# Kernel tuning notes

Hardware: AMD Instinct MI355X
Metric: run time of the kernel (lower is better)

## Reference

```python
import jax, jax.numpy as jnp
import numpy as np
import math

N_HEAD = 16


def _alibi_slopes(n_head):
    def get_slopes(n):
        start = 2.0 ** (-2.0 ** (-(math.log2(n) - 3)))
        return [start * start ** i for i in range(n)]
    if math.log2(n_head).is_integer():
        slopes = get_slopes(n_head)
    else:
        c = 2 ** math.floor(math.log2(n_head))
        slopes = get_slopes(c)
        extra = get_slopes(2 * c)[0::2]
        slopes = slopes + extra[: n_head - c]
    return np.asarray(slopes, dtype=np.float32)


def setup_inputs() -> dict:
    key = jax.random.key(0)
    ks = jax.random.split(key, 9)
    B, S, E = 2, 2048, 1024
    sd = 1.0 / math.sqrt(E)
    inp = {
        "x": jax.random.normal(ks[0], (B, S, E), jnp.float32),
        "Wq": jax.random.uniform(ks[1], (E, E), jnp.float32, -sd, sd),
        "bq": jnp.zeros((E,), jnp.float32),
        "Wk": jax.random.uniform(ks[2], (E, E), jnp.float32, -sd, sd),
        "bk": jnp.zeros((E,), jnp.float32),
        "Wv": jax.random.uniform(ks[3], (E, E), jnp.float32, -sd, sd),
        "bv": jnp.zeros((E,), jnp.float32),
        "Wo": jax.random.uniform(ks[4], (E, E), jnp.float32, -sd, sd),
        "bo": jnp.zeros((E,), jnp.float32),
        "alibi_slopes": jnp.asarray(_alibi_slopes(N_HEAD)),
    }
    return inp


def reference(x, Wq, bq, Wk, bk, Wv, bv, Wo, bo, alibi_slopes):
    B, S, E = x.shape
    H = N_HEAD
    hd = E // H
    scale = hd ** -0.5
    # Linear layers (torch Linear: y = x @ W.T + b)
    Q = (x @ Wq.T + bq).reshape(B, H, S, hd)  # faithful: view, NOT transpose
    K = (x @ Wk.T + bk).reshape(B, H, S, hd)
    V = (x @ Wv.T + bv).reshape(B, H, S, hd)
    scores = jnp.einsum("bhqd,bhkd->bhqk", Q, K) * scale
    pos = jnp.arange(S)
    rel = jnp.abs(pos[None, :] - pos[:, None]).astype(scores.dtype)  # [S,S]
    bias = alibi_slopes[None, :, None, None] * rel[None, None]  # [1,H,S,S]
    scores = scores - bias
    probs = jax.nn.softmax(scores, axis=-1)
    # faithful quirk: keep only head index 1's probs, broadcast to all heads
    probs1 = probs[:, 1:2, :, :]  # [B,1,S,S]
    attn_out = jnp.matmul(probs1, V)  # broadcast -> [B,H,S,hd]
    attn_out = attn_out.reshape(B, S, E)
    out = attn_out @ Wo.T + bo
    return (out, probs1)
```

## Files before the change

### kernel.cpp

```cpp
#include <hip/hip_runtime.h>

typedef __bf16 bf16;
typedef __bf16 bf16_4 __attribute__((ext_vector_type(4)));
typedef __bf16 bf16_8 __attribute__((ext_vector_type(8)));
typedef float f32_4 __attribute__((ext_vector_type(4)));

#define GLDS16(g, l) \
  __builtin_amdgcn_global_load_lds((const __attribute__((address_space(1))) unsigned int*)(g), \
                                   (__attribute__((address_space(3))) unsigned int*)(l), 16, 0, 0)

__global__ __launch_bounds__(256) void convert_all(
    const float* __restrict__ x, const float* __restrict__ wq, const float* __restrict__ wk,
    const float* __restrict__ wv, const float* __restrict__ wo,
    bf16* __restrict__ xb, bf16* __restrict__ wqb, bf16* __restrict__ wkb,
    bf16* __restrict__ wvb, bf16* __restrict__ wob)
{
    for (int i = blockIdx.x * 256 + threadIdx.x; i < 2097152; i += 2048 * 256) {
        const float* s; bf16* d; int off;
        if (i < 1048576) { s = x; d = xb; off = i; }
        else {
            int j = i - 1048576;
            int sel = j >> 18;
            off = j & 262143;
            s = (sel == 0) ? wq : (sel == 1) ? wk : (sel == 2) ? wv : wo;
            d = (sel == 0) ? wqb : (sel == 1) ? wkb : (sel == 2) ? wvb : wob;
        }
        float4 v = reinterpret_cast<const float4*>(s)[off];
        bf16_4 o; o.x = (bf16)v.x; o.y = (bf16)v.y; o.z = (bf16)v.z; o.w = (bf16)v.w;
        reinterpret_cast<bf16_4*>(d)[off] = o;
    }
}

template<int BM, int KU, int NW>
__device__ __forceinline__ void gemm_core(
    const bf16* __restrict__ Ab, int lda,
    const bf16* __restrict__ Wb, int ldw,
    int K, int m0, int n0, int tid,
    bf16* As, bf16* Bs,
    f32_4 (&acc)[(BM == 128) ? 4 : 2][(BM == 128) ? 4 : 2])
{
    constexpr int MI = (BM == 128) ? 4 : 2;
    constexpr int NJ = (BM == 128) ? 4 : 2;
    constexpr int ITA = (BM * 8) / (NW * 64);
    constexpr int ITB = 1024 / (NW * 64);
    const int lane = tid & 63;
    const int wave = tid >> 6;
    const int l15  = lane & 15;
    const int quad = lane >> 4;
    const int WM = (BM == 128) ? (wave >> 1) * 64 : (wave >> 2) * 32;
    const int WN = (BM == 128) ? (wave & 1) * 64 : (wave & 3) * 32;

#pragma unroll
    for (int i = 0; i < MI; i++)
#pragma unroll
        for (int j = 0; j < NJ; j++) acc[i][j] = (f32_4)(0.0f);

    for (int k0 = 0; k0 < K; k0 += 64 * KU) {
#pragma unroll
        for (int ku = 0; ku < KU; ++ku) {
            bf16* Asu = As + ku * BM * 64;
            bf16* Bsu = Bs + ku * 128 * 64;
            int kk = k0 + ku * 64;
#pragma unroll
            for (int it = 0; it < ITA; ++it) {
                int p = wave * (BM * 8 / NW) + it * 64 + lane;
                int r = p >> 3;
                int q = (p & 7) ^ (r & 7);
                GLDS16(Ab + (long long)(m0 + r) * lda + kk + q * 8, Asu + p * 8);
            }
#pragma unroll
            for (int it = 0; it < ITB; ++it) {
                int p = wave * (1024 / NW) + it * 64 + lane;
                int r = p >> 3;
                int q = (p & 7) ^ (r & 7);
                GLDS16(Wb + (long long)(n0 + r) * ldw + kk + q * 8, Bsu + p * 8);
            }
        }
        __syncthreads();

#pragma unroll
        for (int ku = 0; ku < KU; ++ku) {
            bf16* Asu = As + ku * BM * 64;
            bf16* Bsu = Bs + ku * 128 * 64;
#pragma unroll
            for (int kh = 0; kh < 2; ++kh) {
                bf16_8 af[MI], bfr[NJ];
#pragma unroll
                for (int t = 0; t < MI; ++t) {
                    int r = WM + t * 16 + l15;
                    int q = (kh * 4 + quad) ^ (r & 7);
                    af[t] = *reinterpret_cast<const bf16_8*>(&Asu[r * 64 + q * 8]);
                }
#pragma unroll
                for (int j = 0; j < NJ; ++j) {
                    int r = WN + j * 16 + l15;
                    int q = (kh * 4 + quad) ^ (r & 7);
                    bfr[j] = *reinterpret_cast<const bf16_8*>(&Bsu[r * 64 + q * 8]);
                }
#pragma unroll
                for (int i = 0; i < MI; ++i)
#pragma unroll
                    for (int j = 0; j < NJ; ++j)
                        acc[i][j] = __builtin_amdgcn_mfma_f32_16x16x32_bf16(af[i], bfr[j], acc[i][j], 0, 0, 0);
            }
        }
        __syncthreads();
    }
}

__global__ __launch_bounds__(512) void proj_merged(
    const bf16* __restrict__ x_bf,
    const bf16* __restrict__ wv_bf, const float* __restrict__ bv, bf16* __restrict__ v_bf,
    const bf16* __restrict__ wq_bf, const float* __restrict__ bq, bf16* __restrict__ qh1,
    const bf16* __restrict__ wk_bf, const float* __restrict__ bk, bf16* __restrict__ kh1)
{
    __shared__ alignas(16) bf16 As[64 * 64 * 2];
    __shared__ alignas(16) bf16 Bs[128 * 64 * 2];
    const int tid = threadIdx.x;
    const int lane = tid & 63, wave = tid >> 6, l15 = lane & 15, quad = lane >> 4;
    const int n0 = blockIdx.x * 128;

    int m0;
    const bf16* Ab; const bf16* Wb; const float* bvec; bf16* op;
    long long obase;
    int y = blockIdx.y;
    if (y < 64) { m0 = y * 64; Ab = x_bf; Wb = wv_bf; bvec = bv; op = v_bf; obase = 0; }
    else {
        int sub = y - 64;
        int batch = (sub >> 1) & 1;
        int sel = sub >> 2;
        m0 = (sub & 1) * 64;
        Ab = x_bf + (long long)batch * 2097152LL + 131072LL;
        Wb = sel ? wk_bf : wq_bf;
        bvec = sel ? bk : bq;
        op = sel ? kh1 : qh1;
        obase = (long long)batch * 131072LL;
    }

    f32_4 acc[2][2];
    gemm_core<64, 2, 8>(Ab, 1024, Wb, 1024, 1024, m0, n0, tid, As, Bs, acc);

    const int WM = (wave >> 2) * 32;
    const int WN = (wave & 3) * 32;
#pragma unroll
    for (int i = 0; i < 2; i++)
#pragma unroll
        for (int j = 0; j < 2; j++)
#pragma unroll
            for (int rg = 0; rg < 4; rg++) {
                int m = m0 + WM + i * 16 + quad * 4 + rg;
                int n = n0 + WN + j * 16 + l15;
                op[obase + (long long)m * 1024 + n] = (bf16)(acc[i][j][rg] + bvec[n]);
            }
}

__global__ __launch_bounds__(256) void scores_tr(
    const bf16* __restrict__ qh1, const bf16* __restrict__ kh1,
    const float* __restrict__ slopes,
    bf16* __restrict__ pb, float* __restrict__ spart,
    const unsigned short* __restrict__ v_bf, unsigned short* __restrict__ vt)
{
    __shared__ alignas(16) char smem[32768];
    bf16* As = (bf16*)smem;
    bf16* Bs = (bf16*)(smem + 16384);
    const int tid = threadIdx.x;
    const int lane = tid & 63, wave = tid >> 6, l15 = lane & 15, quad = lane >> 4;
    const int n0 = blockIdx.x * 128;
    const int m0 = blockIdx.y * 128;
    const int z  = blockIdx.z;

    f32_4 acc[4][4];
    gemm_core<128, 1, 4>(qh1 + (long long)z * 131072LL, 64,
                         kh1 + (long long)z * 131072LL, 64, 64, m0, n0, tid, As, Bs, acc);

    const int WM = (wave >> 1) * 64;
    const int WN = (wave & 1) * 64;
    const float slope = slopes[1];
    long long obase = (long long)z * 4194304LL;
#pragma unroll
    for (int i = 0; i < 4; i++) {
#pragma unroll
        for (int rg = 0; rg < 4; rg++) {
            int m = m0 + WM + i * 16 + quad * 4 + rg;
            float rowpart = 0.0f;
#pragma unroll
            for (int j = 0; j < 4; j++) {
                int n = n0 + WN + j * 16 + l15;
                float v = acc[i][j][rg] * 0.125f - slope * fabsf((float)(m - n));
                float e = __expf(v);
                rowpart += e;
                pb[obase + (long long)m * 2048 + n] = (bf16)e;
            }
            rowpart += __shfl_xor(rowpart, 1, 64);
            rowpart += __shfl_xor(rowpart, 2, 64);
            rowpart += __shfl_xor(rowpart, 4, 64);
            rowpart += __shfl_xor(rowpart, 8, 64);
            if (l15 == 0)
                spart[((long long)z * 2048 + m) * 32 + (n0 >> 6) + (WN >> 6)] = rowpart;
        }
    }

    unsigned short* tile = (unsigned short*)smem;
    int flat = z * 256 + blockIdx.y * 16 + blockIdx.x;
#pragma unroll
    for (int uu = 0; uu < 2; ++uu) {
        int u = flat * 2 + uu;
        int k0 = (u & 31) * 64, h = (u >> 5) & 15, b = u >> 9;
        const unsigned short* src = v_bf + (long long)b * 2097152LL + (long long)h * 131072LL;
#pragma unroll
        for (int p = 0; p < 8; p++) {
            int idx = tid + p * 256;
            int k = idx >> 5, dc = idx & 31;
            ushort2 w = *reinterpret_cast<const ushort2*>(&src[(long long)(k0 + k) * 64 + dc * 2]);
            tile[(dc * 2) * 66 + k]     = w.x;
            tile[(dc * 2 + 1) * 66 + k] = w.y;
        }
        __syncthreads();
        unsigned short* dst = vt + (long long)b * 2097152LL + (long long)h * 64 * 2048LL + k0;
#pragma unroll
        for (int p = 0; p < 8; p++) {
            int idx = tid + p * 256;
            int d = idx >> 5, kc = idx & 31;
            ushort2 w;
            w.x = tile[d * 66 + kc * 2];
            w.y = tile[d * 66 + kc * 2 + 1];
            *reinterpret_cast<ushort2*>(&dst[(long long)d * 2048 + kc * 2]) = w;
        }
        __syncthreads();
    }
}

__global__ __launch_bounds__(512) void pv_fused(
    const bf16* __restrict__ pb, const bf16* __restrict__ vt,
    const float* __restrict__ spart,
    bf16* __restrict__ attn, float* __restrict__ probs_f)
{
    __shared__ alignas(16) bf16 As[64 * 64 * 2];
    __shared__ alignas(16) bf16 Bs[128 * 64 * 2];
    __shared__ float rs[64];
    const int tid = threadIdx.x;
    const int lane = tid & 63, wave = tid >> 6, l15 = lane & 15, quad = lane >> 4;
    const int nx = blockIdx.x;
    const int n0 = nx * 128;
    const int m0 = blockIdx.y * 64;
    const int z  = blockIdx.z;

    {
        int r = tid >> 3, part = tid & 7;
        const float* sp = spart + ((long long)z * 2048 + m0 + r) * 32 + part * 4;
        float4 a = *reinterpret_cast<const float4*>(sp);
        float v = a.x + a.y + a.z + a.w;
        v += __shfl_xor(v, 1, 64);
        v += __shfl_xor(v, 2, 64);
        v += __shfl_xor(v, 4, 64);
        if (part == 0) rs[r] = 1.0f / v;
    }
    __syncthreads();

    const bf16* Ab = pb + (long long)z * 4194304LL;
    const bf16* Wb = vt + (long long)z * 2097152LL;

    f32_4 acc[2][2];
#pragma unroll
    for (int i = 0; i < 2; i++)
#pragma unroll
        for (int j = 0; j < 2; j++) acc[i][j] = (f32_4)(0.0f);

    const int WM = (wave >> 2) * 32;
    const int WN = (wave & 3) * 32;

    for (int k0 = 0; k0 < 2048; k0 += 128) {
#pragma unroll
        for (int ku = 0; ku < 2; ++ku) {
            bf16* Asu = As + ku * 4096;
            bf16* Bsu = Bs + ku * 8192;
            int kk = k0 + ku * 64;
            {
                int p = wave * 64 + lane;
                int r = p >> 3, q = (p & 7) ^ (r & 7);
                GLDS16(Ab + (long long)(m0 + r) * 2048 + kk + q * 8, Asu + p * 8);
            }
#pragma unroll
            for (int it = 0; it < 2; ++it) {
                int p = wave * 128 + it * 64 + lane;
                int r = p >> 3, q = (p & 7) ^ (r & 7);
                GLDS16(Wb + (long long)(n0 + r) * 2048 + kk + q * 8, Bsu + p * 8);
            }
        }
        __syncthreads();

#pragma unroll
        for (int ku = 0; ku < 2; ++ku) {
            int kk = k0 + ku * 64;
            if ((kk >> 8) == nx) {
                bf16* Asu = As + ku * 4096;
                {
                    int s = tid;
                    int r = s >> 3, q = s & 7;
                    bf16_8 e = *reinterpret_cast<const bf16_8*>(&Asu[r * 64 + (q ^ (r & 7)) * 8]);
                    float inv = rs[r];
                    float4 o0, o1;
                    o0.x = (float)e[0] * inv; o0.y = (float)e[1] * inv;
                    o0.z = (float)e[2] * inv; o0.w = (float)e[3] * inv;
                    o1.x = (float)e[4] * inv; o1.y = (float)e[5] * inv;
                    o1.z = (float)e[6] * inv; o1.w = (float)e[7] * inv;
                    long long base = ((long long)z * 2048 + m0 + r) * 2048 + kk + q * 8;
                    *reinterpret_cast<float4*>(&probs_f[base])     = o0;
                    *reinterpret_cast<float4*>(&probs_f[base + 4]) = o1;
                }
            }
        }

#pragma unroll
        for (int ku = 0; ku < 2; ++ku) {
            bf16* Asu = As + ku * 4096;
            bf16* Bsu = Bs + ku * 8192;
#pragma unroll
            for (int kh = 0; kh < 2; ++kh) {
                bf16_8 af[2], bfr[2];
#pragma unroll
                for (int t = 0; t < 2; ++t) {
                    int r = WM + t * 16 + l15;
                    int q = (kh * 4 + quad) ^ (r & 7);
                    af[t] = *reinterpret_cast<const bf16_8*>(&Asu[r * 64 + q * 8]);
                }
#pragma unroll
                for (int j = 0; j < 2; ++j) {
                    int r = WN + j * 16 + l15;
                    int q = (kh * 4 + quad) ^ (r & 7);
                    bfr[j] = *reinterpret_cast<const bf16_8*>(&Bsu[r * 64 + q * 8]);
                }
#pragma unroll
                for (int i = 0; i < 2; ++i)
#pragma unroll
                    for (int j = 0; j < 2; ++j)
                        acc[i][j] = __builtin_amdgcn_mfma_f32_16x16x32_bf16(af[i], bfr[j], acc[i][j], 0, 0, 0);
            }
        }
        __syncthreads();
    }

    long long obase = (long long)z * 2097152LL;
#pragma unroll
    for (int i = 0; i < 2; i++)
#pragma unroll
        for (int j = 0; j < 2; j++)
#pragma unroll
            for (int rg = 0; rg < 4; rg++) {
                int ml = WM + i * 16 + quad * 4 + rg;
                int m = m0 + ml;
                int n = n0 + WN + j * 16 + l15;
                float v = acc[i][j][rg] * rs[ml];
                long long off = obase + ((long long)(n >> 6)) * 131072LL + (long long)m * 64 + (n & 63);
                attn[off] = (bf16)v;
            }
}

__global__ __launch_bounds__(512) void out_proj(
    const bf16* __restrict__ attn, const bf16* __restrict__ wo_bf,
    const float* __restrict__ bo, float* __restrict__ out_f)
{
    __shared__ alignas(16) bf16 As[64 * 64 * 2];
    __shared__ alignas(16) bf16 Bs[128 * 64 * 2];
    const int tid = threadIdx.x;
    const int lane = tid & 63, wave = tid >> 6, l15 = lane & 15, quad = lane >> 4;
    const int n0 = blockIdx.x * 128;
    const int m0 = blockIdx.y * 64;

    f32_4 acc[2][2];
    gemm_core<64, 2, 8>(attn, 1024, wo_bf, 1024, 1024, m0, n0, tid, As, Bs, acc);

    const int WM = (wave >> 2) * 32;
    const int WN = (wave & 3) * 32;
#pragma unroll
    for (int i = 0; i < 2; i++)
#pragma unroll
        for (int j = 0; j < 2; j++)
#pragma unroll
            for (int rg = 0; rg < 4; rg++) {
                int m = m0 + WM + i * 16 + quad * 4 + rg;
                int n = n0 + WN + j * 16 + l15;
                out_f[(long long)m * 1024 + n] = acc[i][j][rg] + bo[n];
            }
}

extern "C" void kernel_launch(void* const* d_in, const int* in_sizes, int n_in,
                              void* d_out, int out_size, void* d_ws, size_t ws_size,
                              hipStream_t stream) {
    const float* x      = (const float*)d_in[0];
    const float* Wq     = (const float*)d_in[1];
    const float* bq     = (const float*)d_in[2];
    const float* Wk     = (const float*)d_in[3];
    const float* bk     = (const float*)d_in[4];
    const float* Wv     = (const float*)d_in[5];
    const float* bv     = (const float*)d_in[6];
    const float* Wo     = (const float*)d_in[7];
    const float* bo     = (const float*)d_in[8];
    const float* slopes = (const float*)d_in[9];

    char* w = (char*)d_ws;
    bf16* x_bf  = (bf16*)w;  w += 4096LL * 1024 * 2;
    bf16* wq_bf = (bf16*)w;  w += 1024LL * 1024 * 2;
    bf16* wk_bf = (bf16*)w;  w += 1024LL * 1024 * 2;
    bf16* wv_bf = (bf16*)w;  w += 1024LL * 1024 * 2;
    bf16* wo_bf = (bf16*)w;  w += 1024LL * 1024 * 2;
    bf16* qh1   = (bf16*)w;  w += 2LL * 131072 * 2;
    bf16* kh1   = (bf16*)w;  w += 2LL * 131072 * 2;
    bf16* v_bf  = (bf16*)w;  w += 4096LL * 1024 * 2;
    bf16* vt    = (bf16*)w;  w += 2LL * 1024 * 2048 * 2;
    bf16* attn  = (bf16*)w;  w += 4096LL * 1024 * 2;
    bf16* pb    = (bf16*)w;  w += 2LL * 2048 * 2048 * 2;
    float* spart = (float*)w; w += 4096LL * 32 * 4;

    float* out_f   = (float*)d_out;
    float* probs_f = (float*)d_out + 4194304LL;

    convert_all<<<2048, 256, 0, stream>>>(x, Wq, Wk, Wv, Wo, x_bf, wq_bf, wk_bf, wv_bf, wo_bf);

    proj_merged<<<dim3(8, 72, 1), 512, 0, stream>>>(
        x_bf, wv_bf, bv, v_bf, wq_bf, bq, qh1, wk_bf, bk, kh1);

    scores_tr<<<dim3(16, 16, 2), 256, 0, stream>>>(
        qh1, kh1, slopes, pb, spart,
        (const unsigned short*)v_bf, (unsigned short*)vt);

    pv_fused<<<dim3(8, 32, 2), 512, 0, stream>>>(pb, vt, spart, attn, probs_f);

    out_proj<<<dim3(8, 64, 1), 512, 0, stream>>>(attn, wo_bf, bo, out_f);
}
```

Measured before the change: 173.7 us.

## Double-buffer LDS staging in GEMM kernels to overlap loads with MFMA

Replaces the load-all-then-compute loop (two 64-wide K slices per sync) with a ping-pong pipeline that issues global-to-LDS loads for the next 64-wide K tile while MFMAs run on the current one. Partial vmcnt waits and raw s_barrier calls replace full __syncthreads. The change applies to proj_merged, pv_fused and out_proj. In pv_fused the first tile load is issued before the row-sum reduction, and the normalized probs write-out is moved into the per-tile loop. Global memory latency should be hidden better. The risk is correctness if the vmcnt counts or the rs visibility across barriers are wrong.

```diff
diff --git a/kernel.cpp b/kernel.cpp
--- a/kernel.cpp
+++ b/kernel.cpp
@@ -108,14 +108,91 @@
     }
 }
 
+__device__ __forceinline__ void stage_ab64(
+    const bf16* __restrict__ Ab, long long lda,
+    const bf16* __restrict__ Wb, long long ldw,
+    int m0, int n0, int kk, int wave, int lane,
+    bf16* Asb, bf16* Bsb)
+{
+    {
+        int p = wave * 64 + lane;
+        int r = p >> 3, q = (p & 7) ^ (r & 7);
+        GLDS16(Ab + (long long)(m0 + r) * lda + kk + q * 8, Asb + p * 8);
+    }
+#pragma unroll
+    for (int it = 0; it < 2; ++it) {
+        int p = wave * 128 + it * 64 + lane;
+        int r = p >> 3, q = (p & 7) ^ (r & 7);
+        GLDS16(Wb + (long long)(n0 + r) * ldw + kk + q * 8, Bsb + p * 8);
+    }
+}
+
+__device__ __forceinline__ void mma64(
+    const bf16* Asb, const bf16* Bsb, int WM, int WN, int l15, int quad,
+    f32_4 (&acc)[2][2])
+{
+#pragma unroll
+    for (int kh = 0; kh < 2; ++kh) {
+        bf16_8 af[2], bfr[2];
+#pragma unroll
+        for (int t = 0; t < 2; ++t) {
+            int r = WM + t * 16 + l15;
+            int q = (kh * 4 + quad) ^ (r & 7);
+            af[t] = *reinterpret_cast<const bf16_8*>(&Asb[r * 64 + q * 8]);
+        }
+#pragma unroll
+        for (int j = 0; j < 2; ++j) {
+            int r = WN + j * 16 + l15;
+            int q = (kh * 4 + quad) ^ (r & 7);
+            bfr[j] = *reinterpret_cast<const bf16_8*>(&Bsb[r * 64 + q * 8]);
+        }
+#pragma unroll
+        for (int i = 0; i < 2; ++i)
+#pragma unroll
+            for (int j = 0; j < 2; ++j)
+                acc[i][j] = __builtin_amdgcn_mfma_f32_16x16x32_bf16(af[i], bfr[j], acc[i][j], 0, 0, 0);
+    }
+}
+
+template<int NT>
+__device__ __forceinline__ void gemm_db64(
+    const bf16* __restrict__ Ab, long long lda,
+    const bf16* __restrict__ Wb, long long ldw,
+    int m0, int n0, int tid, bf16* As, bf16* Bs,
+    f32_4 (&acc)[2][2])
+{
+    const int lane = tid & 63, wave = tid >> 6, l15 = lane & 15, quad = lane >> 4;
+    const int WM = (wave >> 2) * 32, WN = (wave & 3) * 32;
+#pragma unroll
+    for (int i = 0; i < 2; i++)
+#pragma unroll
+        for (int j = 0; j < 2; j++) acc[i][j] = (f32_4)(0.0f);
+
+    stage_ab64(Ab, lda, Wb, ldw, m0, n0, 0, wave, lane, As, Bs);
+    for (int t = 0; t < NT; ++t) {
+        const int cur = t & 1;
+        if (t + 1 < NT) {
+            stage_ab64(Ab, lda, Wb, ldw, m0, n0, (t + 1) * 64, wave, lane,
+                       As + (cur ^ 1) * 4096, Bs + (cur ^ 1) * 8192);
+            asm volatile("s_waitcnt vmcnt(3)" ::: "memory");
+        } else {
+            asm volatile("s_waitcnt vmcnt(0)" ::: "memory");
+        }
+        __builtin_amdgcn_s_barrier();
+        mma64(As + cur * 4096, Bs + cur * 8192, WM, WN, l15, quad, acc);
+        asm volatile("s_waitcnt lgkmcnt(0)" ::: "memory");
+        __builtin_amdgcn_s_barrier();
+    }
+}
+
 __global__ __launch_bounds__(512) void proj_merged(
     const bf16* __restrict__ x_bf,
     const bf16* __restrict__ wv_bf, const float* __restrict__ bv, bf16* __restrict__ v_bf,
     const bf16* __restrict__ wq_bf, const float* __restrict__ bq, bf16* __restrict__ qh1,
     const bf16* __restrict__ wk_bf, const float* __restrict__ bk, bf16* __restrict__ kh1)
 {
-    __shared__ alignas(16) bf16 As[64 * 64 * 2];
-    __shared__ alignas(16) bf16 Bs[128 * 64 * 2];
+    __shared__ alignas(16) bf16 As[2 * 4096];
+    __shared__ alignas(16) bf16 Bs[2 * 8192];
     const int tid = threadIdx.x;
     const int lane = tid & 63, wave = tid >> 6, l15 = lane & 15, quad = lane >> 4;
     const int n0 = blockIdx.x * 128;
@@ -138,7 +215,7 @@
     }
 
     f32_4 acc[2][2];
-    gemm_core<64, 2, 8>(Ab, 1024, Wb, 1024, 1024, m0, n0, tid, As, Bs, acc);
+    gemm_db64<16>(Ab, 1024, Wb, 1024, m0, n0, tid, As, Bs, acc);
 
     const int WM = (wave >> 2) * 32;
     const int WN = (wave & 3) * 32;
@@ -235,8 +312,8 @@
     const float* __restrict__ spart,
     bf16* __restrict__ attn, float* __restrict__ probs_f)
 {
-    __shared__ alignas(16) bf16 As[64 * 64 * 2];
-    __shared__ alignas(16) bf16 Bs[128 * 64 * 2];
+    __shared__ alignas(16) bf16 As[2 * 4096];
+    __shared__ alignas(16) bf16 Bs[2 * 8192];
     __shared__ float rs[64];
     const int tid = threadIdx.x;
     const int lane = tid & 63, wave = tid >> 6, l15 = lane & 15, quad = lane >> 4;
@@ -244,6 +321,12 @@
     const int n0 = nx * 128;
     const int m0 = blockIdx.y * 64;
     const int z  = blockIdx.z;
+    const int WM = (wave >> 2) * 32, WN = (wave & 3) * 32;
+
+    const bf16* Ab = pb + (long long)z * 4194304LL;
+    const bf16* Wb = vt + (long long)z * 2097152LL;
+
+    stage_ab64(Ab, 2048, Wb, 2048, m0, n0, 0, wave, lane, As, Bs);
 
     {
         int r = tid >> 3, part = tid & 7;
@@ -255,10 +338,6 @@
         v += __shfl_xor(v, 4, 64);
         if (part == 0) rs[r] = 1.0f / v;
     }
-    __syncthreads();
-
-    const bf16* Ab = pb + (long long)z * 4194304LL;
-    const bf16* Wb = vt + (long long)z * 2097152LL;
 
     f32_4 acc[2][2];
 #pragma unroll
@@ -266,78 +345,37 @@
 #pragma unroll
         for (int j = 0; j < 2; j++) acc[i][j] = (f32_4)(0.0f);
 
-    const int WM = (wave >> 2) * 32;
-    const int WN = (wave & 3) * 32;
-
-    for (int k0 = 0; k0 < 2048; k0 += 128) {
-#pragma unroll
-        for (int ku = 0; ku < 2; ++ku) {
-            bf16* Asu = As + ku * 4096;
-            bf16* Bsu = Bs + ku * 8192;
-            int kk = k0 + ku * 64;
-            {
-                int p = wave * 64 + lane;
-                int r = p >> 3, q = (p & 7) ^ (r & 7);
-                GLDS16(Ab + (long long)(m0 + r) * 2048 + kk + q * 8, Asu + p * 8);
-            }
-#pragma unroll
-            for (int it = 0; it < 2; ++it) {
-                int p = wave * 128 + it * 64 + lane;
-                int r = p >> 3, q = (p & 7) ^ (r & 7);
-                GLDS16(Wb + (long long)(n0 + r) * 2048 + kk + q * 8, Bsu + p * 8);
-            }
-        }
-        __syncthreads();
-
-#pragma unroll
-        for (int ku = 0; ku < 2; ++ku) {
-            int kk = k0 + ku * 64;
-            if ((kk >> 8) == nx) {
-                bf16* Asu = As + ku * 4096;
-                {
-                    int s = tid;
-                    int r = s >> 3, q = s & 7;
-                    bf16_8 e = *reinterpret_cast<const bf16_8*>(&Asu[r * 64 + (q ^ (r & 7)) * 8]);
-                    float inv = rs[r];
-                    float4 o0, o1;
-                    o0.x = (float)e[0] * inv; o0.y = (float)e[1] * inv;
-                    o0.z = (float)e[2] * inv; o0.w = (float)e[3] * inv;
-                    o1.x = (float)e[4] * inv; o1.y = (float)e[5] * inv;
-                    o1.z = (float)e[6] * inv; o1.w = (float)e[7] * inv;
-                    long long base = ((long long)z * 2048 + m0 + r) * 2048 + kk + q * 8;
-                    *reinterpret_cast<float4*>(&probs_f[base])     = o0;
-                    *reinterpret_cast<float4*>(&probs_f[base + 4]) = o1;
-                }
-            }
-        }
-
-#pragma unroll
-        for (int ku = 0; ku < 2; ++ku) {
-            bf16* Asu = As + ku * 4096;
-            bf16* Bsu = Bs + ku * 8192;
-#pragma unroll
-            for (int kh = 0; kh < 2; ++kh) {
-                bf16_8 af[2], bfr[2];
-#pragma unroll
-                for (int t = 0; t < 2; ++t) {
-                    int r = WM + t * 16 + l15;
-                    int q = (kh * 4 + quad) ^ (r & 7);
-                    af[t] = *reinterpret_cast<const bf16_8*>(&Asu[r * 64 + q * 8]);
-                }
-#pragma unroll
-                for (int j = 0; j < 2; ++j) {
-                    int r = WN + j * 16 + l15;
-                    int q = (kh * 4 + quad) ^ (r & 7);
-                    bfr[j] = *reinterpret_cast<const bf16_8*>(&Bsu[r * 64 + q * 8]);
-                }
-#pragma unroll
-                for (int i = 0; i < 2; ++i)
-#pragma unroll
-                    for (int j = 0; j < 2; ++j)
-                        acc[i][j] = __builtin_amdgcn_mfma_f32_16x16x32_bf16(af[i], bfr[j], acc[i][j], 0, 0, 0);
-            }
-        }
-        __syncthreads();
+    for (int t = 0; t < 32; ++t) {
+        const int cur = t & 1;
+        if (t + 1 < 32) {
+            stage_ab64(Ab, 2048, Wb, 2048, m0, n0, (t + 1) * 64, wave, lane,
+                       As + (cur ^ 1) * 4096, Bs + (cur ^ 1) * 8192);
+            asm volatile("s_waitcnt vmcnt(3)" ::: "memory");
+        } else {
+            asm volatile("s_waitcnt vmcnt(0)" ::: "memory");
+        }
+        __builtin_amdgcn_s_barrier();
+
+        if ((t >> 2) == nx) {
+            const bf16* Asu = As + cur * 4096;
+            int s = tid;
+            int r = s >> 3, q = s & 7;
+            bf16_8 e = *reinterpret_cast<const bf16_8*>(&Asu[r * 64 + (q ^ (r & 7)) * 8]);
+            float inv = rs[r];
+            float4 o0, o1;
+            o0.x = (float)e[0] * inv; o0.y = (float)e[1] * inv;
+            o0.z = (float)e[2] * inv; o0.w = (float)e[3] * inv;
+            o1.x = (float)e[4] * inv; o1.y = (float)e[5] * inv;
+            o1.z = (float)e[6] * inv; o1.w = (float)e[7] * inv;
+            long long base = ((long long)z * 2048 + m0 + r) * 2048 + t * 64 + q * 8;
+            *reinterpret_cast<float4*>(&probs_f[base])     = o0;
+            *reinterpret_cast<float4*>(&probs_f[base + 4]) = o1;
+        }
+
+        mma64(As + cur * 4096, Bs + cur * 8192, WM, WN, l15, quad, acc);
+
+        asm volatile("s_waitcnt lgkmcnt(0)" ::: "memory");
+        __builtin_amdgcn_s_barrier();
     }
 
     long long obase = (long long)z * 2097152LL;
@@ -360,15 +398,15 @@
     const bf16* __restrict__ attn, const bf16* __restrict__ wo_bf,
     const float* __restrict__ bo, float* __restrict__ out_f)
 {
-    __shared__ alignas(16) bf16 As[64 * 64 * 2];
-    __shared__ alignas(16) bf16 Bs[128 * 64 * 2];
+    __shared__ alignas(16) bf16 As[2 * 4096];
+    __shared__ alignas(16) bf16 Bs[2 * 8192];
     const int tid = threadIdx.x;
     const int lane = tid & 63, wave = tid >> 6, l15 = lane & 15, quad = lane >> 4;
     const int n0 = blockIdx.x * 128;
     const int m0 = blockIdx.y * 64;
 
     f32_4 acc[2][2];
-    gemm_core<64, 2, 8>(attn, 1024, wo_bf, 1024, 1024, m0, n0, tid, As, Bs, acc);
+    gemm_db64<16>(attn, 1024, wo_bf, 1024, m0, n0, tid, As, Bs, acc);
 
     const int WM = (wave >> 2) * 32;
     const int WN = (wave & 3) * 32;
```

Result: no change. 173.4 us (-0.2%).
